# Performance work log

Hardware: AMD Instinct MI355X
Metric: run time of the kernel (lower is better)

Reference implementation:

```python
import jax, jax.numpy as jnp
import numpy as np

B, D, N, K = 4, 1024, 2048, 1024
INIT_STD = 0.05  # keras 'random_normal' initializer default stddev


def setup_inputs() -> dict:
    key = jax.random.key(0)
    kx, kq, kk, kv, ko = jax.random.split(key, 5)
    inputs = jax.random.normal(kx, (B, D, N), dtype=jnp.float32)
    W_Q = jax.random.normal(kq, (K, D), dtype=jnp.float32) * INIT_STD
    W_K = jax.random.normal(kk, (K, D), dtype=jnp.float32) * INIT_STD
    W_V = jax.random.normal(kv, (K, D), dtype=jnp.float32) * INIT_STD
    W_O = jax.random.normal(ko, (K, D), dtype=jnp.float32) * INIT_STD
    return {"inputs": inputs, "W_Q": W_Q, "W_K": W_K, "W_V": W_V, "W_O": W_O}


def reference(inputs, W_Q, W_K, W_V, W_O):
    # inputs: (b, d, n) -- feature-major layout, sequence on the last axis.
    b, d, n = inputs.shape
    # Q/K projections fused into a single bilinear form: (W_Q x_i) . (W_K x_j)
    # logits[b, i, j] = x[:, i]^T W_Q^T W_K x[:, j]
    q = jnp.einsum('kd,bdi->bki', W_Q, inputs)          # (b, k, n)
    kk = jnp.einsum('kd,bdj->bkj', W_K, inputs)         # (b, k, n)
    logits = jnp.einsum('bki,bkj->bij', q, kk)          # (b, n, n)
    # Causal mask D: -inf strictly above the diagonal (query i attends j <= i).
    causal = jnp.tril(jnp.ones((n, n), dtype=bool))
    logits = jnp.where(causal, logits, -jnp.inf)
    A = jax.nn.softmax(logits, axis=-1)                 # (b, n_q, n_k)
    # context[:, :, i] = sum_t x[:, :, t] * A[i, t]
    ctx = jnp.einsum('bet,bit->bei', inputs, A)         # (b, d, n)
    # Residual + fused V/O projection: x + W_O^T W_V x A
    out = inputs + jnp.einsum('kd,ke,bei->bdi', W_O, W_V, ctx)
    return out
```

## Files before the change

### kernel.cpp

```cpp
#include <hip/hip_runtime.h>
#include <hip/hip_bf16.h>
#include <math.h>

#define BB 4
#define DD 1024
#define NN 2048
#define KK 1024
#define NT128 16
#define NTRI 136
#define TRI_ELEMS 16384

typedef __attribute__((ext_vector_type(4))) float f32x4;
typedef __attribute__((ext_vector_type(8))) short bfrag;

typedef __attribute__((address_space(1))) const unsigned int gu32;
typedef __attribute__((address_space(3))) unsigned int lu32;

__device__ __forceinline__ void async16(const void* g, void* l) {
  __builtin_amdgcn_global_load_lds((gu32*)g, (lu32*)l, 16, 0, 0);
}

__device__ __forceinline__ ushort f2b(float f) {
  union { float f; unsigned u; } c; c.f = f;
  unsigned u = c.u + 0x7fffu + ((c.u >> 16) & 1u);
  return (ushort)(u >> 16);
}
__device__ __forceinline__ float b2f(ushort h) {
  union { unsigned u; float f; } c; c.u = ((unsigned)h) << 16;
  return c.f;
}

__global__ __launch_bounds__(256) void transpose_split(
    const float* __restrict__ x, ushort* __restrict__ xhi,
    ushort* __restrict__ xTh, ushort* __restrict__ xTl) {
  const int b = blockIdx.z;
  const int n0 = blockIdx.x * 32, d0 = blockIdx.y * 32;
  const int tx = threadIdx.x, ty = threadIdx.y;
  __shared__ float tile[32][33];
  const float* xb = x + (long)b * DD * NN;
  ushort* xhb = xhi + (long)b * DD * NN;
#pragma unroll
  for (int r = 0; r < 4; ++r) {
    const int dl = ty + r * 8;
    const float v = xb[(long)(d0 + dl) * NN + n0 + tx];
    tile[dl][tx] = v;
    xhb[(long)(d0 + dl) * NN + n0 + tx] = f2b(v);
  }
  __syncthreads();
#pragma unroll
  for (int r = 0; r < 4; ++r) {
    const int nl = ty + r * 8;
    const float v = tile[tx][nl];
    const ushort h = f2b(v);
    const long o = (long)b * NN * DD + (long)(n0 + nl) * DD + d0 + tx;
    xTh[o] = h;
    xTl[o] = f2b(v - b2f(h));
  }
}

__global__ __launch_bounds__(256) void wtrans4(
    const float* __restrict__ WQ, const float* __restrict__ WK,
    const float* __restrict__ WV, const float* __restrict__ WO,
    ushort* __restrict__ qh, ushort* __restrict__ ql,
    ushort* __restrict__ kh, ushort* __restrict__ kl_,
    ushort* __restrict__ vh, ushort* __restrict__ oh) {
  const int z = blockIdx.z;
  const float* W = (z == 0) ? WQ : (z == 1) ? WK : (z == 2) ? WV : WO;
  ushort* Th = (z == 0) ? qh : (z == 1) ? kh : (z == 2) ? vh : oh;
  ushort* Tl = (z == 0) ? ql : (z == 1) ? kl_ : nullptr;
  const int k0 = blockIdx.x * 32, d0 = blockIdx.y * 32;
  const int tx = threadIdx.x, ty = threadIdx.y;
  __shared__ float tile[32][33];
#pragma unroll
  for (int r = 0; r < 4; ++r) {
    const int kl = ty + r * 8;
    tile[kl][tx] = W[(long)(k0 + kl) * DD + d0 + tx];
  }
  __syncthreads();
#pragma unroll
  for (int r = 0; r < 4; ++r) {
    const int dl = ty + r * 8;
    const float v = tile[tx][dl];
    const ushort h = f2b(v);
    const long o = (long)(d0 + dl) * KK + k0 + tx;
    Th[o] = h;
    if (Tl) Tl[o] = f2b(v - b2f(h));
  }
}

template <int SPLIT, int TRIA, int STORE, int SWIZ>
__global__ __launch_bounds__(256) void gemm_mfma(
    const ushort* __restrict__ Ah, const ushort* __restrict__ Al,
    const ushort* __restrict__ Bh, const ushort* __restrict__ Bl,
    void* __restrict__ C0, void* __restrict__ C1, const float* __restrict__ Res,
    int K, int lda, int ldb, int ldc,
    long bA, long bB, long bC, long bR) {
  extern __shared__ ushort smem[];
  ushort* sAh = smem;
  ushort* sBh = smem + (SPLIT ? 8192 : 4096);
  ushort* sAl = SPLIT ? smem + 4096 : nullptr;
  ushort* sBl = SPLIT ? smem + 12288 : nullptr;

  int b, m0, n0, tiC = 0;
  if (SWIZ == 2) {
    const int g = (blockIdx.x & 7) * 68 + (blockIdx.x >> 3);
    b = g / NTRI;
    int t = g - b * NTRI;
    int ti = 0;
    while ((ti + 1) * (ti + 2) / 2 <= t) ++ti;
    const int tj = t - ti * (ti + 1) / 2;
    m0 = ti * 128; n0 = tj * 128; tiC = t;
  } else if (SWIZ == 1) {
    const int g = (blockIdx.x & 7) * 64 + (blockIdx.x >> 3);
    const int P = g >> 3;
    b = P >> 4;
    m0 = (P & 15) * 128;
    n0 = (g & 7) * 128;
  } else {
    b = blockIdx.z; m0 = blockIdx.y * 128; n0 = blockIdx.x * 128;
  }
  const int kmax = TRIA ? (m0 + 128) : K;
  int triA0 = 0;
  if (TRIA) { const int ti = m0 >> 7; triA0 = ti * (ti + 1) / 2; }

  const ushort* A_h = Ah + (long)b * bA;
  const ushort* B_h = Bh + (long)b * bB;
  const ushort* A_l = SPLIT ? Al + (long)b * bA : nullptr;
  const ushort* B_l = SPLIT ? Bl + (long)b * bB : nullptr;

  const int tid = threadIdx.x;
  const int lane = tid & 63, wave = tid >> 6;
  const int wm = (wave & 1) * 64, wn = (wave >> 1) * 64;
  const int r16 = lane & 15, quad = lane >> 4;

  f32x4 acc[4][4];
#pragma unroll
  for (int i = 0; i < 4; ++i)
#pragma unroll
    for (int j = 0; j < 4; ++j) acc[i][j] = (f32x4){0.f, 0.f, 0.f, 0.f};

  for (int k0 = 0; k0 < kmax; k0 += 32) {
    __syncthreads();
    {
      const int kc = (lane & 3) * 8;
#pragma unroll
      for (int c = 0; c < 2; ++c) {
        const int seg = wave * 2 + c;
        const int row = seg * 16 + (lane >> 2);
        long aoff;
        if (TRIA)
          aoff = (long)(triA0 + (k0 >> 7)) * TRI_ELEMS + (long)row * 128 + (k0 & 127) + kc;
        else
          aoff = (long)(m0 + row) * lda + k0 + kc;
        const long boff = (long)(n0 + row) * ldb + k0 + kc;
        async16(A_h + aoff, sAh + seg * 512);
        async16(B_h + boff, sBh + seg * 512);
        if (SPLIT) {
          async16(A_l + aoff, sAl + seg * 512);
          async16(B_l + boff, sBl + seg * 512);
        }
      }
    }
    __syncthreads();

    bfrag ah[4], bh[4], al[4], bl[4];
#pragma unroll
    for (int t4 = 0; t4 < 4; ++t4) {
      ah[t4] = *(const bfrag*)&sAh[(wm + t4 * 16 + r16) * 32 + quad * 8];
      bh[t4] = *(const bfrag*)&sBh[(wn + t4 * 16 + r16) * 32 + quad * 8];
      if (SPLIT) {
        al[t4] = *(const bfrag*)&sAl[(wm + t4 * 16 + r16) * 32 + quad * 8];
        bl[t4] = *(const bfrag*)&sBl[(wn + t4 * 16 + r16) * 32 + quad * 8];
      }
    }
#pragma unroll
    for (int mt = 0; mt < 4; ++mt)
#pragma unroll
      for (int nt = 0; nt < 4; ++nt) {
        acc[mt][nt] = __builtin_amdgcn_mfma_f32_16x16x32_bf16(ah[mt], bh[nt], acc[mt][nt], 0, 0, 0);
        if (SPLIT) {
          acc[mt][nt] = __builtin_amdgcn_mfma_f32_16x16x32_bf16(ah[mt], bl[nt], acc[mt][nt], 0, 0, 0);
          acc[mt][nt] = __builtin_amdgcn_mfma_f32_16x16x32_bf16(al[mt], bh[nt], acc[mt][nt], 0, 0, 0);
        }
      }
  }

#pragma unroll
  for (int mt = 0; mt < 4; ++mt)
#pragma unroll
    for (int nt = 0; nt < 4; ++nt)
#pragma unroll
      for (int reg = 0; reg < 4; ++reg) {
        const int ml = wm + mt * 16 + quad * 4 + reg;
        const int nl = wn + nt * 16 + r16;
        const float v = acc[mt][nt][reg];
        if (STORE == 0) {
          ushort* Ch = (ushort*)C0 + (long)b * bC;
          ushort* Cl = (ushort*)C1 + (long)b * bC;
          const long o = (long)(m0 + ml) * ldc + n0 + nl;
          const ushort h = f2b(v);
          Ch[o] = h;
          Cl[o] = f2b(v - b2f(h));
        } else if (STORE == 1) {
          float* C = (float*)C0 + (long)b * bC + (long)tiC * TRI_ELEMS;
          C[ml * 128 + nl] = v;
        } else if (STORE == 2) {
          ushort* C = (ushort*)C0 + (long)b * bC;
          C[(long)(m0 + ml) * ldc + n0 + nl] = f2b(v);
        } else {
          float* C = (float*)C0 + (long)b * bC;
          const float* R = Res + (long)b * bR;
          const long o = (long)(m0 + ml) * ldc + n0 + nl;
          C[o] = R[o] + v;
        }
      }
}

__global__ __launch_bounds__(256) void softmax_tri(
    const float* __restrict__ L, ushort* __restrict__ Aout) {
  const int row = blockIdx.x;
  const int b = row >> 11, i = row & (NN - 1);
  const int ti = i >> 7, ml = i & 127;
  const long base = (long)b * ((long)NTRI * TRI_ELEMS);
  const int trib = ti * (ti + 1) / 2;
  const int len = i + 1;
  const int tot = (ti + 1) * 128;
  const int tid = threadIdx.x;
  __shared__ float red[256];
  float vv[8];
  float m = -INFINITY;
#pragma unroll
  for (int u = 0; u < 8; ++u) {
    const int j = tid + u * 256;
    if (j < len) {
      const float v = L[base + (long)(trib + (j >> 7)) * TRI_ELEMS + ml * 128 + (j & 127)];
      vv[u] = v;
      m = fmaxf(m, v);
    }
  }
  red[tid] = m; __syncthreads();
  for (int s = 128; s; s >>= 1) { if (tid < s) red[tid] = fmaxf(red[tid], red[tid + s]); __syncthreads(); }
  m = red[0]; __syncthreads();
  float sum = 0.f;
#pragma unroll
  for (int u = 0; u < 8; ++u) {
    const int j = tid + u * 256;
    if (j < len) { const float e = __expf(vv[u] - m); vv[u] = e; sum += e; }
  }
  red[tid] = sum; __syncthreads();
  for (int s = 128; s; s >>= 1) { if (tid < s) red[tid] += red[tid + s]; __syncthreads(); }
  const float inv = 1.f / red[0];
#pragma unroll
  for (int u = 0; u < 8; ++u) {
    const int j = tid + u * 256;
    if (j < tot) {
      const ushort o = (j < len) ? f2b(vv[u] * inv) : (ushort)0;
      Aout[base + (long)(trib + (j >> 7)) * TRI_ELEMS + ml * 128 + (j & 127)] = o;
    }
  }
}

extern "C" void kernel_launch(void* const* d_in, const int* in_sizes, int n_in,
                              void* d_out, int out_size, void* d_ws, size_t ws_size,
                              hipStream_t stream) {
  const float* x = (const float*)d_in[0];
  const float* WQ = (const float*)d_in[1];
  const float* WK = (const float*)d_in[2];
  const float* WV = (const float*)d_in[3];
  const float* WO = (const float*)d_in[4];
  float* out = (float*)d_out;

  const long XE = (long)BB * DD * NN;
  const long WE = (long)DD * KK;
  ushort* x_hi = (ushort*)d_ws;
  ushort* xTh = x_hi + XE;
  ushort* xTl = xTh + XE;
  ushort* wqT_h = xTl + XE;
  ushort* wqT_l = wqT_h + WE;
  ushort* wkT_h = wqT_l + WE;
  ushort* wkT_l = wkT_h + WE;
  ushort* wvT_h = wkT_l + WE;
  ushort* woT_h = wvT_h + WE;
  ushort* mqk_h = woT_h + WE;
  ushort* mqk_l = mqk_h + WE;
  ushort* mov_h = mqk_l + WE;
  ushort* tTh = mov_h + WE;
  ushort* tTl = tTh + XE;
  float* logits = (float*)(tTl + XE);
  ushort* A_tri = tTh;
  ushort* ctxT = (ushort*)logits;
  const long TRIB = (long)NTRI * TRI_ELEMS;
  const long XB = XE / BB;

  transpose_split<<<dim3(NN / 32, DD / 32, BB), dim3(32, 8), 0, stream>>>(x, x_hi, xTh, xTl);
  wtrans4<<<dim3(KK / 32, DD / 32, 4), dim3(32, 8), 0, stream>>>(
      WQ, WK, WV, WO, wqT_h, wqT_l, wkT_h, wkT_l, wvT_h, woT_h);

  gemm_mfma<1, 0, 0, 0><<<dim3(DD / 128, DD / 128, 1), 256, 32768, stream>>>(
      wqT_h, wqT_l, wkT_h, wkT_l, mqk_h, mqk_l, nullptr,
      KK, KK, KK, DD, 0, 0, 0, 0);
  gemm_mfma<0, 0, 2, 0><<<dim3(DD / 128, DD / 128, 1), 256, 16384, stream>>>(
      woT_h, nullptr, wvT_h, nullptr, mov_h, nullptr, nullptr,
      KK, KK, KK, DD, 0, 0, 0, 0);

  gemm_mfma<1, 0, 0, 1><<<dim3(512), 256, 32768, stream>>>(
      xTh, xTl, mqk_h, mqk_l, tTh, tTl, nullptr,
      DD, DD, DD, DD, XB, 0, XB, 0);

  gemm_mfma<1, 0, 1, 2><<<dim3(BB * NTRI), 256, 32768, stream>>>(
      xTh, xTl, tTh, tTl, logits, nullptr, nullptr,
      DD, DD, DD, 0, XB, XB, TRIB, 0);

  softmax_tri<<<dim3(BB * NN), 256, 0, stream>>>(logits, A_tri);

  gemm_mfma<0, 1, 2, 1><<<dim3(512), 256, 16384, stream>>>(
      A_tri, nullptr, x_hi, nullptr, ctxT, nullptr, nullptr,
      NN, 0, NN, DD, TRIB, XB, XB, 0);

  gemm_mfma<0, 0, 3, 0><<<dim3(NN / 128, DD / 128, BB), 256, 16384, stream>>>(
      mov_h, nullptr, ctxT, nullptr, out, nullptr, x,
      DD, DD, DD, NN, 0, XB, XB, XB);
}
```

Measured before the change: 391.6 us.

## Merge prep kernels, fuse weight GEMMs with 64x64 tiles, swizzle LDS reads

The two transpose/split kernels become one prep launch, and the two 1024x1024 weight-product GEMMs become a single launch with 64x64 tiles. That gives 512 blocks instead of two launches of 64 blocks each, which better fills the GPU's compute units. An XOR swizzle is also added to the LDS staging and fragment reads in the main GEMM template, aimed at reducing bank conflicts. The smaller tiles lower per-block data reuse, and the swizzle has to match exactly between the async write and the read or results will be wrong.

```diff
diff --git a/kernel.cpp b/kernel.cpp
--- a/kernel.cpp
+++ b/kernel.cpp
@@ -30,62 +30,152 @@
   return c.f;
 }
 
-__global__ __launch_bounds__(256) void transpose_split(
-    const float* __restrict__ x, ushort* __restrict__ xhi,
-    ushort* __restrict__ xTh, ushort* __restrict__ xTl) {
-  const int b = blockIdx.z;
-  const int n0 = blockIdx.x * 32, d0 = blockIdx.y * 32;
-  const int tx = threadIdx.x, ty = threadIdx.y;
-  __shared__ float tile[32][33];
-  const float* xb = x + (long)b * DD * NN;
-  ushort* xhb = xhi + (long)b * DD * NN;
-#pragma unroll
-  for (int r = 0; r < 4; ++r) {
-    const int dl = ty + r * 8;
-    const float v = xb[(long)(d0 + dl) * NN + n0 + tx];
-    tile[dl][tx] = v;
-    xhb[(long)(d0 + dl) * NN + n0 + tx] = f2b(v);
-  }
-  __syncthreads();
-#pragma unroll
-  for (int r = 0; r < 4; ++r) {
-    const int nl = ty + r * 8;
-    const float v = tile[tx][nl];
-    const ushort h = f2b(v);
-    const long o = (long)b * NN * DD + (long)(n0 + nl) * DD + d0 + tx;
-    xTh[o] = h;
-    xTl[o] = f2b(v - b2f(h));
-  }
-}
-
-__global__ __launch_bounds__(256) void wtrans4(
+
+__global__ __launch_bounds__(256) void prep(
+    const float* __restrict__ x,
     const float* __restrict__ WQ, const float* __restrict__ WK,
     const float* __restrict__ WV, const float* __restrict__ WO,
+    ushort* __restrict__ xhi, ushort* __restrict__ xTh, ushort* __restrict__ xTl,
     ushort* __restrict__ qh, ushort* __restrict__ ql,
     ushort* __restrict__ kh, ushort* __restrict__ kl_,
     ushort* __restrict__ vh, ushort* __restrict__ oh) {
   const int z = blockIdx.z;
-  const float* W = (z == 0) ? WQ : (z == 1) ? WK : (z == 2) ? WV : WO;
-  ushort* Th = (z == 0) ? qh : (z == 1) ? kh : (z == 2) ? vh : oh;
-  ushort* Tl = (z == 0) ? ql : (z == 1) ? kl_ : nullptr;
-  const int k0 = blockIdx.x * 32, d0 = blockIdx.y * 32;
   const int tx = threadIdx.x, ty = threadIdx.y;
   __shared__ float tile[32][33];
-#pragma unroll
-  for (int r = 0; r < 4; ++r) {
-    const int kl = ty + r * 8;
-    tile[kl][tx] = W[(long)(k0 + kl) * DD + d0 + tx];
-  }
-  __syncthreads();
-#pragma unroll
-  for (int r = 0; r < 4; ++r) {
-    const int dl = ty + r * 8;
-    const float v = tile[tx][dl];
-    const ushort h = f2b(v);
-    const long o = (long)(d0 + dl) * KK + k0 + tx;
-    Th[o] = h;
-    if (Tl) Tl[o] = f2b(v - b2f(h));
-  }
+  if (z < 4) {
+    const int b = z;
+    const int n0 = blockIdx.x * 32, d0 = blockIdx.y * 32;
+    const float* xb = x + (long)b * DD * NN;
+    ushort* xhb = xhi + (long)b * DD * NN;
+#pragma unroll
+    for (int r = 0; r < 4; ++r) {
+      const int dl = ty + r * 8;
+      const float v = xb[(long)(d0 + dl) * NN + n0 + tx];
+      tile[dl][tx] = v;
+      xhb[(long)(d0 + dl) * NN + n0 + tx] = f2b(v);
+    }
+    __syncthreads();
+#pragma unroll
+    for (int r = 0; r < 4; ++r) {
+      const int nl = ty + r * 8;
+      const float v = tile[tx][nl];
+      const ushort h = f2b(v);
+      const long o = (long)b * NN * DD + (long)(n0 + nl) * DD + d0 + tx;
+      xTh[o] = h;
+      xTl[o] = f2b(v - b2f(h));
+    }
+  } else {
+    const int w = (z - 4) * 2 + (blockIdx.x >> 5);
+    const float* W = (w == 0) ? WQ : (w == 1) ? WK : (w == 2) ? WV : WO;
+    ushort* Th = (w == 0) ? qh : (w == 1) ? kh : (w == 2) ? vh : oh;
+    ushort* Tl = (w == 0) ? ql : (w == 1) ? kl_ : nullptr;
+    const int k0 = (blockIdx.x & 31) * 32, d0 = blockIdx.y * 32;
+#pragma unroll
+    for (int r = 0; r < 4; ++r) {
+      const int kl = ty + r * 8;
+      tile[kl][tx] = W[(long)(k0 + kl) * DD + d0 + tx];
+    }
+    __syncthreads();
+#pragma unroll
+    for (int r = 0; r < 4; ++r) {
+      const int dl = ty + r * 8;
+      const float v = tile[tx][dl];
+      const ushort h = f2b(v);
+      const long o = (long)(d0 + dl) * KK + k0 + tx;
+      Th[o] = h;
+      if (Tl) Tl[o] = f2b(v - b2f(h));
+    }
+  }
+}
+
+__global__ __launch_bounds__(256) void gemm_w(
+    const ushort* __restrict__ qh, const ushort* __restrict__ ql,
+    const ushort* __restrict__ kh, const ushort* __restrict__ kl_,
+    const ushort* __restrict__ vh, const ushort* __restrict__ oh,
+    ushort* __restrict__ mqk_h, ushort* __restrict__ mqk_l,
+    ushort* __restrict__ mov_h) {
+  extern __shared__ ushort smem[];
+  ushort* sAh = smem;
+  ushort* sAl = smem + 2048;
+  ushort* sBh = smem + 4096;
+  ushort* sBl = smem + 6144;
+
+  const int id = blockIdx.x;
+  const int half = id >> 8;
+  const int t = id & 255;
+  const int m0 = (t >> 4) * 64, n0 = (t & 15) * 64;
+  const ushort* A_h = half ? oh : qh;
+  const ushort* B_h = half ? vh : kh;
+
+  const int tid = threadIdx.x;
+  const int lane = tid & 63, wave = tid >> 6;
+  const int wm = (wave & 1) * 32, wn = (wave >> 1) * 32;
+  const int r16 = lane & 15, quad = lane >> 4;
+  const int kc = ((lane & 3) ^ ((lane >> 3) & 3)) * 8;
+  const int srow = lane >> 2;
+
+  f32x4 acc[2][2];
+#pragma unroll
+  for (int i = 0; i < 2; ++i)
+#pragma unroll
+    for (int j = 0; j < 2; ++j) acc[i][j] = (f32x4){0.f, 0.f, 0.f, 0.f};
+
+  for (int k0 = 0; k0 < KK; k0 += 32) {
+    __syncthreads();
+    {
+      const int row = wave * 16 + srow;
+      const long aoff = (long)(m0 + row) * KK + k0 + kc;
+      const long boff = (long)(n0 + row) * KK + k0 + kc;
+      async16(A_h + aoff, sAh + wave * 512);
+      async16(B_h + boff, sBh + wave * 512);
+      if (half == 0) {
+        async16(ql + aoff, sAl + wave * 512);
+        async16(kl_ + boff, sBl + wave * 512);
+      }
+    }
+    __syncthreads();
+
+    const int sw = (r16 >> 1) & 3;
+    bfrag ah[2], bh[2], al[2], bl[2];
+#pragma unroll
+    for (int t2 = 0; t2 < 2; ++t2) {
+      ah[t2] = *(const bfrag*)&sAh[(wm + t2 * 16 + r16) * 32 + (quad ^ sw) * 8];
+      bh[t2] = *(const bfrag*)&sBh[(wn + t2 * 16 + r16) * 32 + (quad ^ sw) * 8];
+      if (half == 0) {
+        al[t2] = *(const bfrag*)&sAl[(wm + t2 * 16 + r16) * 32 + (quad ^ sw) * 8];
+        bl[t2] = *(const bfrag*)&sBl[(wn + t2 * 16 + r16) * 32 + (quad ^ sw) * 8];
+      }
+    }
+#pragma unroll
+    for (int mt = 0; mt < 2; ++mt)
+#pragma unroll
+      for (int nt = 0; nt < 2; ++nt) {
+        acc[mt][nt] = __builtin_amdgcn_mfma_f32_16x16x32_bf16(ah[mt], bh[nt], acc[mt][nt], 0, 0, 0);
+        if (half == 0) {
+          acc[mt][nt] = __builtin_amdgcn_mfma_f32_16x16x32_bf16(ah[mt], bl[nt], acc[mt][nt], 0, 0, 0);
+          acc[mt][nt] = __builtin_amdgcn_mfma_f32_16x16x32_bf16(al[mt], bh[nt], acc[mt][nt], 0, 0, 0);
+        }
+      }
+  }
+
+#pragma unroll
+  for (int mt = 0; mt < 2; ++mt)
+#pragma unroll
+    for (int nt = 0; nt < 2; ++nt)
+#pragma unroll
+      for (int reg = 0; reg < 4; ++reg) {
+        const int ml = wm + mt * 16 + quad * 4 + reg;
+        const int nl = wn + nt * 16 + r16;
+        const float v = acc[mt][nt][reg];
+        const long o = (long)(m0 + ml) * DD + n0 + nl;
+        if (half == 0) {
+          const ushort h = f2b(v);
+          mqk_h[o] = h;
+          mqk_l[o] = f2b(v - b2f(h));
+        } else {
+          mov_h[o] = f2b(v);
+        }
+      }
 }
 
 template <int SPLIT, int TRIA, int STORE, int SWIZ>
@@ -132,6 +222,7 @@
   const int lane = tid & 63, wave = tid >> 6;
   const int wm = (wave & 1) * 64, wn = (wave >> 1) * 64;
   const int r16 = lane & 15, quad = lane >> 4;
+  const int kc = ((lane & 3) ^ ((lane >> 3) & 3)) * 8;
 
   f32x4 acc[4][4];
 #pragma unroll
@@ -142,7 +233,6 @@
   for (int k0 = 0; k0 < kmax; k0 += 32) {
     __syncthreads();
     {
-      const int kc = (lane & 3) * 8;
 #pragma unroll
       for (int c = 0; c < 2; ++c) {
         const int seg = wave * 2 + c;
@@ -163,14 +253,15 @@
     }
     __syncthreads();
 
+    const int sw = (r16 >> 1) & 3;
     bfrag ah[4], bh[4], al[4], bl[4];
 #pragma unroll
     for (int t4 = 0; t4 < 4; ++t4) {
-      ah[t4] = *(const bfrag*)&sAh[(wm + t4 * 16 + r16) * 32 + quad * 8];
-      bh[t4] = *(const bfrag*)&sBh[(wn + t4 * 16 + r16) * 32 + quad * 8];
+      ah[t4] = *(const bfrag*)&sAh[(wm + t4 * 16 + r16) * 32 + (quad ^ sw) * 8];
+      bh[t4] = *(const bfrag*)&sBh[(wn + t4 * 16 + r16) * 32 + (quad ^ sw) * 8];
       if (SPLIT) {
-        al[t4] = *(const bfrag*)&sAl[(wm + t4 * 16 + r16) * 32 + quad * 8];
-        bl[t4] = *(const bfrag*)&sBl[(wn + t4 * 16 + r16) * 32 + quad * 8];
+        al[t4] = *(const bfrag*)&sAl[(wm + t4 * 16 + r16) * 32 + (quad ^ sw) * 8];
+        bl[t4] = *(const bfrag*)&sBl[(wn + t4 * 16 + r16) * 32 + (quad ^ sw) * 8];
       }
     }
 #pragma unroll
@@ -292,16 +383,12 @@
   const long TRIB = (long)NTRI * TRI_ELEMS;
   const long XB = XE / BB;
 
-  transpose_split<<<dim3(NN / 32, DD / 32, BB), dim3(32, 8), 0, stream>>>(x, x_hi, xTh, xTl);
-  wtrans4<<<dim3(KK / 32, DD / 32, 4), dim3(32, 8), 0, stream>>>(
-      WQ, WK, WV, WO, wqT_h, wqT_l, wkT_h, wkT_l, wvT_h, woT_h);
-
-  gemm_mfma<1, 0, 0, 0><<<dim3(DD / 128, DD / 128, 1), 256, 32768, stream>>>(
-      wqT_h, wqT_l, wkT_h, wkT_l, mqk_h, mqk_l, nullptr,
-      KK, KK, KK, DD, 0, 0, 0, 0);
-  gemm_mfma<0, 0, 2, 0><<<dim3(DD / 128, DD / 128, 1), 256, 16384, stream>>>(
-      woT_h, nullptr, wvT_h, nullptr, mov_h, nullptr, nullptr,
-      KK, KK, KK, DD, 0, 0, 0, 0);
+  prep<<<dim3(64, 32, 6), dim3(32, 8), 0, stream>>>(
+      x, WQ, WK, WV, WO, x_hi, xTh, xTl,
+      wqT_h, wqT_l, wkT_h, wkT_l, wvT_h, woT_h);
+
+  gemm_w<<<dim3(512), 256, 16384, stream>>>(
+      wqT_h, wqT_l, wkT_h, wkT_l, wvT_h, woT_h, mqk_h, mqk_l, mov_h);
 
   gemm_mfma<1, 0, 0, 1><<<dim3(512), 256, 32768, stream>>>(
       xTh, xTl, mqk_h, mqk_l, tTh, tTl, nullptr,
```

New measurement: 352.9 us. 9.9% less time.
